# Kernel tuning notes

Hardware: AMD Instinct MI355X
Metric: run time of the kernel (lower is better)

Reference implementation:

```python
import jax, jax.numpy as jnp
import numpy as np

N_NODES = 50000
N_EDGES = 800000
N_GRAPHS = 500
BN_EPS = 1e-5
DIMS = [128, 256, 256, 256, 256, 256, 256]  # in, conv1..5, concat


def setup_inputs() -> dict:
    key = jax.random.key(0)
    ks = jax.random.split(key, 16)
    inp = {
        "x": jax.random.normal(ks[0], (N_NODES, DIMS[0]), jnp.float32),
        "edge_index": jax.random.randint(ks[1], (2, N_EDGES), 0, N_NODES, dtype=jnp.int64),
        "batch": jnp.sort(jax.random.randint(ks[2], (N_NODES,), 0, N_GRAPHS, dtype=jnp.int64)),
    }
    for i in range(6):
        fin, fout = DIMS[i], DIMS[i + 1]
        inp[f"W{i+1}"] = jax.random.normal(ks[3 + i], (fin, fout), jnp.float32) / np.sqrt(fin)
        inp[f"b{i+1}"] = jnp.zeros((fout,), jnp.float32)
    for i in range(5):
        inp[f"gamma{i+1}"] = jnp.ones((DIMS[i + 1],), jnp.float32)
        inp[f"beta{i+1}"] = jnp.zeros((DIMS[i + 1],), jnp.float32)
    return inp


def _gcn_conv(x, src, dst, dinv, W, b):
    # PyG GCNConv: add self-loops, symmetric norm D^-1/2 (A+I) D^-1/2, x@W then aggregate, + bias
    xw = x @ W  # [N, Fout]
    norm = dinv[src] * dinv[dst]  # [E]
    agg = jax.ops.segment_sum(norm[:, None] * xw[src], dst, num_segments=N_NODES)
    agg = agg + (dinv * dinv)[:, None] * xw  # self-loop contribution
    return agg + b


def _bn(x, gamma, beta):
    # BatchNorm1d, training-mode batch statistics (biased variance, as torch)
    m = x.mean(axis=0)
    v = x.var(axis=0)
    return gamma * (x - m) * jax.lax.rsqrt(v + BN_EPS) + beta


def reference(x, edge_index, batch,
              W1, b1, W2, b2, W3, b3, W4, b4, W5, b5, W6, b6,
              gamma1, beta1, gamma2, beta2, gamma3, beta3, gamma4, beta4, gamma5, beta5):
    src, dst = edge_index[0], edge_index[1]
    # degree of A + I (counted over destination nodes)
    deg = jnp.zeros((N_NODES,), x.dtype).at[dst].add(1.0) + 1.0
    dinv = jax.lax.rsqrt(deg)
    h = x
    convs = [(W1, b1), (W2, b2), (W3, b3), (W4, b4), (W5, b5)]
    bns = [(gamma1, beta1), (gamma2, beta2), (gamma3, beta3), (gamma4, beta4), (gamma5, beta5)]
    for (W, b), (g, be) in zip(convs, bns):
        h = jax.nn.relu(_gcn_conv(h, src, dst, dinv, W, b))
        h = _bn(h, g, be)
    h = jax.nn.relu(_gcn_conv(h, src, dst, dinv, W6, b6))
    # global_add_pool; dropout is identity in eval mode
    return jax.ops.segment_sum(h, batch, num_segments=N_GRAPHS)
```

## Files before the change

kernel.cpp:

```cpp
#include <hip/hip_runtime.h>

#define N_NODES 50000
#define N_EDGES 800000
#define N_GRAPHS 500
#define BN_EPS 1e-5f
#define F 256
#define SCAN_BLOCKS ((N_NODES + 255) / 256)
#define NPART 64

typedef short short8 __attribute__((ext_vector_type(8)));
typedef short short4v __attribute__((ext_vector_type(4)));
typedef float f32x4 __attribute__((ext_vector_type(4)));
typedef _Float16 h16x8 __attribute__((ext_vector_type(8)));

__global__ void k_hist(const int* __restrict__ dst, int* __restrict__ cnt) {
    int e0 = (blockIdx.x * blockDim.x + threadIdx.x) * 4;
    if (e0 >= N_EDGES) return;
    int4 d4 = *reinterpret_cast<const int4*>(&dst[e0]);
    atomicAdd(&cnt[d4.x], 1);
    atomicAdd(&cnt[d4.y], 1);
    atomicAdd(&cnt[d4.z], 1);
    atomicAdd(&cnt[d4.w], 1);
}

__global__ void k_dinv(const int* __restrict__ cnt, float* __restrict__ dinv) {
    int n = blockIdx.x * blockDim.x + threadIdx.x;
    if (n < N_NODES) dinv[n] = rsqrtf((float)cnt[n] + 1.0f);
}

__global__ void k_scan1(const int* __restrict__ cnt, int* __restrict__ rowptr,
                        int* __restrict__ bsum) {
    __shared__ int s[256];
    int tid = threadIdx.x;
    int i = blockIdx.x * 256 + tid;
    int v = (i < N_NODES) ? cnt[i] : 0;
    s[tid] = v;
    __syncthreads();
    for (int off = 1; off < 256; off <<= 1) {
        int add = (tid >= off) ? s[tid - off] : 0;
        __syncthreads();
        s[tid] += add;
        __syncthreads();
    }
    if (i < N_NODES) rowptr[i] = s[tid] - v;
    if (tid == 255) bsum[blockIdx.x] = s[255];
}

__global__ void k_scan2(int* __restrict__ bsum) {
    __shared__ int s[256];
    int tid = threadIdx.x;
    int v = (tid < SCAN_BLOCKS) ? bsum[tid] : 0;
    s[tid] = v;
    __syncthreads();
    for (int off = 1; off < 256; off <<= 1) {
        int add = (tid >= off) ? s[tid - off] : 0;
        __syncthreads();
        s[tid] += add;
        __syncthreads();
    }
    if (tid < SCAN_BLOCKS) bsum[tid] = s[tid] - v;
}

__global__ void k_scan3(int* __restrict__ rowptr, const int* __restrict__ bsum) {
    int i = blockIdx.x * 256 + threadIdx.x;
    if (i < N_NODES) rowptr[i] += bsum[blockIdx.x];
    if (i == 0) rowptr[N_NODES] = N_EDGES;
}

__global__ void k_scatter(const int* __restrict__ src, const int* __restrict__ dst,
                          const float* __restrict__ dinv, int* __restrict__ fillptr,
                          int2* __restrict__ epair) {
    int e0 = (blockIdx.x * blockDim.x + threadIdx.x) * 4;
    if (e0 >= N_EDGES) return;
    int4 s4 = *reinterpret_cast<const int4*>(&src[e0]);
    int4 d4 = *reinterpret_cast<const int4*>(&dst[e0]);
    int ss[4] = {s4.x, s4.y, s4.z, s4.w};
    int dd[4] = {d4.x, d4.y, d4.z, d4.w};
    #pragma unroll
    for (int j = 0; j < 4; ++j) {
        float norm = dinv[ss[j]] * dinv[dd[j]];
        int slot = atomicAdd(&fillptr[dd[j]], 1);
        epair[slot] = make_int2(ss[j], __float_as_int(norm));
    }
}

__global__ void k_pack(const float* __restrict__ W, short* __restrict__ hi,
                       short* __restrict__ lo, int K) {
    int idx = blockIdx.x * 256 + threadIdx.x;
    if (idx >= 256 * K) return;
    int n = idx / K, k = idx - n * K;
    float f = W[(size_t)k * 256 + n];
    unsigned u = __builtin_bit_cast(unsigned, f);
    hi[idx] = (short)(u >> 16);
    float hf = __builtin_bit_cast(float, u & 0xFFFF0000u);
    lo[idx] = (short)(__builtin_bit_cast(unsigned, f - hf) >> 16);
}

__global__ __launch_bounds__(256)
void k_wfold(const float* __restrict__ W, const float* __restrict__ stats,
             const float* __restrict__ gamma, const float* __restrict__ beta,
             short* __restrict__ hi, short* __restrict__ lo,
             float* __restrict__ rowvec) {
    __shared__ float red[256];
    const int n = blockIdx.x;
    const int k = threadIdx.x;
    float s = 0.f, q = 0.f;
    for (int p = 0; p < NPART; ++p) {
        s += stats[(size_t)p * 512 + k];
        q += stats[(size_t)p * 512 + 256 + k];
    }
    float m = s * (1.0f / N_NODES);
    float var = q * (1.0f / N_NODES) - m * m;
    float mulk = gamma[k] * rsqrtf(var + BN_EPS);
    float addk = beta[k] - m * mulk;
    float w = W[(size_t)k * 256 + n];
    float f = w * mulk;
    unsigned u = __builtin_bit_cast(unsigned, f);
    hi[(size_t)n * 256 + k] = (short)(u >> 16);
    float hf = __builtin_bit_cast(float, u & 0xFFFF0000u);
    lo[(size_t)n * 256 + k] = (short)(__builtin_bit_cast(unsigned, f - hf) >> 16);
    red[k] = addk * w;
    __syncthreads();
    for (int off = 128; off > 0; off >>= 1) {
        if (k < off) red[k] += red[k + off];
        __syncthreads();
    }
    if (k == 0) rowvec[n] = red[0];
}

__global__ void k_splitx(const float* __restrict__ x, short* __restrict__ hi,
                         short* __restrict__ lo) {
    int idx = blockIdx.x * 256 + threadIdx.x;
    if (idx >= N_NODES * 32) return;
    float4 v = reinterpret_cast<const float4*>(x)[idx];
    float vv[4] = {v.x, v.y, v.z, v.w};
    short4v h4, l4;
    #pragma unroll
    for (int j = 0; j < 4; ++j) {
        unsigned u = __builtin_bit_cast(unsigned, vv[j]);
        h4[j] = (short)(u >> 16);
        float hf = __builtin_bit_cast(float, u & 0xFFFF0000u);
        l4[j] = (short)(__builtin_bit_cast(unsigned, vv[j] - hf) >> 16);
    }
    *reinterpret_cast<short4v*>(&hi[(size_t)idx * 4]) = h4;
    *reinterpret_cast<short4v*>(&lo[(size_t)idx * 4]) = l4;
}

#define BK 32
__global__ __launch_bounds__(256)
void k_gemm_mfma(const short* __restrict__ Ahi, const short* __restrict__ Alo,
                 const short* __restrict__ Bhi, const short* __restrict__ Blo,
                 _Float16* __restrict__ C, int M, int K) {
    __shared__ unsigned As[2][2][128 * 16];
    const int tid  = threadIdx.x;
    const int lane = tid & 63;
    const int w    = tid >> 6;
    const int wr   = (w >> 1) * 64;
    const int wc   = (w & 1) * 64;
    const int bid  = blockIdx.x;
    const int bx   = (bid >> 4) * 8 + (bid & 7);
    const int by   = (bid >> 3) & 1;
    const int brow = bx * 128;
    const int bcol = by * 128;

    f32x4 acc[4][4];
    #pragma unroll
    for (int m = 0; m < 4; ++m)
        #pragma unroll
        for (int n = 0; n < 4; ++n) acc[m][n] = (f32x4){0.f, 0.f, 0.f, 0.f};

    const int lr = tid >> 1;
    const int lk = (tid & 1) * 16;
    const int grow = brow + lr;
    const bool rowok = grow < M;
    const short* Ahp = Ahi + (size_t)grow * K + lk;
    const short* Alp = Alo + (size_t)grow * K + lk;
    const int NS = K / BK;

    uint4 ph0, ph1, pl0, pl1;
    auto load_pf = [&](int s) {
        if (rowok) {
            ph0 = *reinterpret_cast<const uint4*>(Ahp + s * BK);
            ph1 = *reinterpret_cast<const uint4*>(Ahp + s * BK + 8);
            pl0 = *reinterpret_cast<const uint4*>(Alp + s * BK);
            pl1 = *reinterpret_cast<const uint4*>(Alp + s * BK + 8);
        } else {
            ph0 = ph1 = pl0 = pl1 = make_uint4(0, 0, 0, 0);
        }
    };

    const int sw  = (lr >> 1) & 3;
    const int c0  = (tid & 1) * 2;
    const int off0 = lr * 16 + ((c0 ^ sw) << 2);
    const int off1 = lr * 16 + (((c0 + 1) ^ sw) << 2);

    load_pf(0);
    *reinterpret_cast<uint4*>(&As[0][0][off0]) = ph0;
    *reinterpret_cast<uint4*>(&As[0][0][off1]) = ph1;
    *reinterpret_cast<uint4*>(&As[0][1][off0]) = pl0;
    *reinterpret_cast<uint4*>(&As[0][1][off1]) = pl1;

    for (int s = 0; s < NS; ++s) {
        const int cur = s & 1;
        if (s + 1 < NS) load_pf(s + 1);
        __syncthreads();

        short8 bh[4], bl[4];
        const int kb = s * BK + (lane >> 4) * 8;
        #pragma unroll
        for (int n = 0; n < 4; ++n) {
            int col = bcol + wc + n * 16 + (lane & 15);
            bh[n] = *reinterpret_cast<const short8*>(Bhi + (size_t)col * K + kb);
            bl[n] = *reinterpret_cast<const short8*>(Blo + (size_t)col * K + kb);
        }
        #pragma unroll
        for (int m = 0; m < 4; ++m) {
            int row = wr + m * 16 + (lane & 15);
            int c = lane >> 4;
            int sw2 = (row >> 1) & 3;
            const unsigned* ph = &As[cur][0][row * 16 + ((c ^ sw2) << 2)];
            const unsigned* pl = &As[cur][1][row * 16 + ((c ^ sw2) << 2)];
            short8 ah = *reinterpret_cast<const short8*>(ph);
            short8 al = *reinterpret_cast<const short8*>(pl);
            #pragma unroll
            for (int n = 0; n < 4; ++n) {
                acc[m][n] = __builtin_amdgcn_mfma_f32_16x16x32_bf16(ah, bh[n], acc[m][n], 0, 0, 0);
                acc[m][n] = __builtin_amdgcn_mfma_f32_16x16x32_bf16(al, bh[n], acc[m][n], 0, 0, 0);
                acc[m][n] = __builtin_amdgcn_mfma_f32_16x16x32_bf16(ah, bl[n], acc[m][n], 0, 0, 0);
            }
        }
        if (s + 1 < NS) {
            *reinterpret_cast<uint4*>(&As[cur ^ 1][0][off0]) = ph0;
            *reinterpret_cast<uint4*>(&As[cur ^ 1][0][off1]) = ph1;
            *reinterpret_cast<uint4*>(&As[cur ^ 1][1][off0]) = pl0;
            *reinterpret_cast<uint4*>(&As[cur ^ 1][1][off1]) = pl1;
        }
    }

    #pragma unroll
    for (int m = 0; m < 4; ++m) {
        #pragma unroll
        for (int n = 0; n < 4; ++n) {
            int col = bcol + wc + n * 16 + (lane & 15);
            #pragma unroll
            for (int j = 0; j < 4; ++j) {
                int row = brow + wr + m * 16 + (lane >> 4) * 4 + j;
                if (row < M) C[(size_t)row * 256 + col] = (_Float16)acc[m][n][j];
            }
        }
    }
}

#define BATCH 8
template<int MODE>
__global__ __launch_bounds__(256)
void k_agg2(const _Float16* __restrict__ xw, const float* __restrict__ dinv,
            const int* __restrict__ rowptr, const int2* __restrict__ epair,
            const float* __restrict__ bias, const float* __restrict__ rowvec,
            short* __restrict__ hhi, short* __restrict__ hlo,
            float* __restrict__ hf32, float* __restrict__ stats) {
    __shared__ float red[2][4][256];
    const int lane = threadIdx.x & 63;
    const int wave = threadIdx.x >> 6;
    const int half = lane >> 5;
    const int fl   = lane & 31;
    const int n    = blockIdx.x * 4 + wave;

    const h16x8* xw8 = reinterpret_cast<const h16x8*>(xw);

    float acc[8];
    float wsum;
    if (half == 0) {
        float d = dinv[n];
        float sl = d * d;
        h16x8 sv = xw8[(size_t)n * 32 + fl];
        #pragma unroll
        for (int j = 0; j < 8; ++j) acc[j] = sl * (float)sv[j];
        wsum = sl;
    } else {
        #pragma unroll
        for (int j = 0; j < 8; ++j) acc[j] = 0.f;
        wsum = 0.f;
    }

    const int beg = rowptr[n], end = rowptr[n + 1];
    int i = beg + half;

    if (i < end) {
        int ecur[BATCH]; float wcur[BATCH];
        #pragma unroll
        for (int k = 0; k < BATCH; ++k) {
            int idx = i + 2 * k;
            bool ok = idx < end;
            int2 p = epair[ok ? idx : (end - 1)];
            ecur[k] = p.x;
            wcur[k] = ok ? __int_as_float(p.y) : 0.f;
        }
        while (true) {
            h16x8 r[BATCH];
            #pragma unroll
            for (int k = 0; k < BATCH; ++k)
                r[k] = xw8[(size_t)ecur[k] * 32 + fl];

            int inext = i + 2 * BATCH;
            bool more = inext < end;
            int enxt[BATCH]; float wnxt[BATCH];
            if (more) {
                #pragma unroll
                for (int k = 0; k < BATCH; ++k) {
                    int idx = inext + 2 * k;
                    bool ok = idx < end;
                    int2 p = epair[ok ? idx : (end - 1)];
                    enxt[k] = p.x;
                    wnxt[k] = ok ? __int_as_float(p.y) : 0.f;
                }
            }
            #pragma unroll
            for (int k = 0; k < BATCH; ++k) {
                wsum += wcur[k];
                #pragma unroll
                for (int j = 0; j < 8; ++j)
                    acc[j] = fmaf(wcur[k], (float)r[k][j], acc[j]);
            }
            if (!more) break;
            i = inext;
            #pragma unroll
            for (int k = 0; k < BATCH; ++k) { ecur[k] = enxt[k]; wcur[k] = wnxt[k]; }
        }
    }

    #pragma unroll
    for (int j = 0; j < 8; ++j) acc[j] += __shfl_xor(acc[j], 32, 64);
    wsum += __shfl_xor(wsum, 32, 64);

    if (half == 0) {
        float4 b0 = *reinterpret_cast<const float4*>(&bias[fl * 8]);
        float4 b1 = *reinterpret_cast<const float4*>(&bias[fl * 8 + 4]);
        float4 r0 = *reinterpret_cast<const float4*>(&rowvec[fl * 8]);
        float4 r1 = *reinterpret_cast<const float4*>(&rowvec[fl * 8 + 4]);
        float bv[8] = {b0.x, b0.y, b0.z, b0.w, b1.x, b1.y, b1.z, b1.w};
        float rv[8] = {r0.x, r0.y, r0.z, r0.w, r1.x, r1.y, r1.z, r1.w};
        #pragma unroll
        for (int j = 0; j < 8; ++j)
            acc[j] = fmaxf(acc[j] + fmaf(wsum, rv[j], bv[j]), 0.f);

        if (MODE == 0) {
            unsigned hw[4], lw[4];
            #pragma unroll
            for (int p = 0; p < 4; ++p) {
                float f0 = acc[2 * p], f1 = acc[2 * p + 1];
                unsigned u0 = __builtin_bit_cast(unsigned, f0);
                unsigned u1 = __builtin_bit_cast(unsigned, f1);
                hw[p] = (u1 & 0xFFFF0000u) | (u0 >> 16);
                float h0 = __builtin_bit_cast(float, u0 & 0xFFFF0000u);
                float h1 = __builtin_bit_cast(float, u1 & 0xFFFF0000u);
                lw[p] = (__builtin_bit_cast(unsigned, f1 - h1) & 0xFFFF0000u) |
                        (__builtin_bit_cast(unsigned, f0 - h0) >> 16);
            }
            *reinterpret_cast<uint4*>(&hhi[(size_t)n * 256 + fl * 8]) =
                make_uint4(hw[0], hw[1], hw[2], hw[3]);
            *reinterpret_cast<uint4*>(&hlo[(size_t)n * 256 + fl * 8]) =
                make_uint4(lw[0], lw[1], lw[2], lw[3]);
            float4 o0 = make_float4(acc[0], acc[1], acc[2], acc[3]);
            float4 o1 = make_float4(acc[4], acc[5], acc[6], acc[7]);
            float4 q0 = make_float4(acc[0]*acc[0], acc[1]*acc[1], acc[2]*acc[2], acc[3]*acc[3]);
            float4 q1 = make_float4(acc[4]*acc[4], acc[5]*acc[5], acc[6]*acc[6], acc[7]*acc[7]);
            *reinterpret_cast<float4*>(&red[0][wave][fl * 8])     = o0;
            *reinterpret_cast<float4*>(&red[0][wave][fl * 8 + 4]) = o1;
            *reinterpret_cast<float4*>(&red[1][wave][fl * 8])     = q0;
            *reinterpret_cast<float4*>(&red[1][wave][fl * 8 + 4]) = q1;
        } else {
            *reinterpret_cast<float4*>(&hf32[(size_t)n * 256 + fl * 8]) =
                make_float4(acc[0], acc[1], acc[2], acc[3]);
            *reinterpret_cast<float4*>(&hf32[(size_t)n * 256 + fl * 8 + 4]) =
                make_float4(acc[4], acc[5], acc[6], acc[7]);
        }
    }

    if (MODE == 0) {
        __syncthreads();
        int t = threadIdx.x;
        float s = red[0][0][t] + red[0][1][t] + red[0][2][t] + red[0][3][t];
        float q = red[1][0][t] + red[1][1][t] + red[1][2][t] + red[1][3][t];
        float* part = stats + (size_t)(blockIdx.x & (NPART - 1)) * 512;
        atomicAdd(&part[t], s);
        atomicAdd(&part[256 + t], q);
    }
}

template<int ROWS>
__global__ __launch_bounds__(256)
void k_pool(const float* __restrict__ h, const int* __restrict__ batch,
            float* __restrict__ out) {
    const int f = threadIdx.x;
    const int r0 = blockIdx.x * ROWS;
    float acc = 0.f;
    int cur = -1;
    for (int i = 0; i < ROWS; ++i) {
        int n = r0 + i;
        if (n >= N_NODES) break;
        int g = batch[n];
        float v = h[(size_t)n * F + f];
        if (g != cur) {
            if (cur >= 0) atomicAdd(&out[(size_t)cur * F + f], acc);
            cur = g; acc = v;
        } else {
            acc += v;
        }
    }
    if (cur >= 0) atomicAdd(&out[(size_t)cur * F + f], acc);
}

extern "C" void kernel_launch(void* const* d_in, const int* in_sizes, int n_in,
                              void* d_out, int out_size, void* d_ws, size_t ws_size,
                              hipStream_t stream) {
    const float* x     = (const float*)d_in[0];
    const int*   ei    = (const int*)d_in[1];
    const int*   batch = (const int*)d_in[2];
    const float* W[6], *bias[6], *gamma[5], *beta[5];
    for (int i = 0; i < 6; ++i) {
        W[i]    = (const float*)d_in[3 + 2 * i];
        bias[i] = (const float*)d_in[4 + 2 * i];
    }
    for (int i = 0; i < 5; ++i) {
        gamma[i] = (const float*)d_in[15 + 2 * i];
        beta[i]  = (const float*)d_in[16 + 2 * i];
    }
    float* out = (float*)d_out;

    char* ws = (char*)d_ws;
    size_t off = 0;
    auto alloc = [&](size_t bytes) {
        void* p = ws + off;
        off = (off + bytes + 255) & ~(size_t)255;
        return p;
    };
    int*   cnt      = (int*)  alloc(N_NODES * 4);
    int*   rowptr   = (int*)  alloc((N_NODES + 1) * 4);
    int*   fillptr  = (int*)  alloc(N_NODES * 4);
    int*   bsum     = (int*)  alloc(256 * 4);
    float* dinv     = (float*)alloc(N_NODES * 4);
    int2*  epair    = (int2*) alloc((size_t)N_EDGES * 8);
    float* rowvec   = (float*)alloc(F * 4);
    float* statsAll = (float*)alloc((size_t)5 * NPART * 512 * 4);
    short* Whi[6]; short* Wlo[6];
    for (int l = 0; l < 6; ++l) {
        int K = (l == 0) ? 128 : 256;
        Whi[l] = (short*)alloc((size_t)256 * K * 2);
        Wlo[l] = (short*)alloc((size_t)256 * K * 2);
    }
    short* xhi = (short*)alloc((size_t)N_NODES * 128 * 2);
    short* xlo = (short*)alloc((size_t)N_NODES * 128 * 2);
    short* hhi = (short*)alloc((size_t)N_NODES * F * 2);
    short* hlo = (short*)alloc((size_t)N_NODES * F * 2);
    _Float16* xw   = (_Float16*)alloc((size_t)N_NODES * F * 2);
    float*    hfin = (float*)   alloc((size_t)N_NODES * F * 4);

    const int* src = ei;
    const int* dst = ei + N_EDGES;

    hipMemsetAsync(cnt, 0, N_NODES * 4, stream);
    hipMemsetAsync(out, 0, (size_t)N_GRAPHS * F * 4, stream);
    hipMemsetAsync(rowvec, 0, F * 4, stream);
    hipMemsetAsync(statsAll, 0, (size_t)5 * NPART * 512 * 4, stream);
    k_hist<<<(N_EDGES / 4 + 255) / 256, 256, 0, stream>>>(dst, cnt);
    k_dinv<<<(N_NODES + 255) / 256, 256, 0, stream>>>(cnt, dinv);
    k_scan1<<<SCAN_BLOCKS, 256, 0, stream>>>(cnt, rowptr, bsum);
    k_scan2<<<1, 256, 0, stream>>>(bsum);
    k_scan3<<<SCAN_BLOCKS, 256, 0, stream>>>(rowptr, bsum);
    hipMemcpyAsync(fillptr, rowptr, N_NODES * 4, hipMemcpyDeviceToDevice, stream);
    k_scatter<<<(N_EDGES / 4 + 255) / 256, 256, 0, stream>>>(src, dst, dinv, fillptr, epair);
    k_pack<<<(256 * 128 + 255) / 256, 256, 0, stream>>>(W[0], Whi[0], Wlo[0], 128);
    k_splitx<<<(N_NODES * 32 + 255) / 256, 256, 0, stream>>>(x, xhi, xlo);

    const int aggGrid = N_NODES / 4;
    for (int l = 0; l < 6; ++l) {
        const int K = (l == 0) ? 128 : 256;
        const short* Ah = (l == 0) ? xhi : hhi;
        const short* Al = (l == 0) ? xlo : hlo;
        k_gemm_mfma<<<784, 256, 0, stream>>>(Ah, Al, Whi[l], Wlo[l], xw, N_NODES, K);

        if (l < 5) {
            float* stats = statsAll + (size_t)l * NPART * 512;
            k_agg2<0><<<aggGrid, 256, 0, stream>>>(xw, dinv, rowptr, epair,
                                                   bias[l], rowvec, hhi, hlo,
                                                   nullptr, stats);
            k_wfold<<<256, 256, 0, stream>>>(W[l + 1], stats, gamma[l], beta[l],
                                             Whi[l + 1], Wlo[l + 1], rowvec);
        } else {
            k_agg2<1><<<aggGrid, 256, 0, stream>>>(xw, dinv, rowptr, epair,
                                                   bias[l], rowvec, nullptr, nullptr,
                                                   hfin, nullptr);
            k_pool<128><<<(N_NODES + 127) / 128, 256, 0, stream>>>(hfin, batch, out);
        }
    }
}
```

Measured before the change: 1.076 ms.

## Split aggregation into feature chunks with one node per 4-lane group

```diff
diff --git a/kernel.cpp b/kernel.cpp
--- a/kernel.cpp
+++ b/kernel.cpp
@@ -7,6 +7,9 @@
 #define F 256
 #define SCAN_BLOCKS ((N_NODES + 255) / 256)
 #define NPART 64
+#define NCHUNK 8
+#define NODES_PER_BLOCK 64
+#define NODE_BLOCKS ((N_NODES + NODES_PER_BLOCK - 1) / NODES_PER_BLOCK)
 
 typedef short short8 __attribute__((ext_vector_type(8)));
 typedef short short4v __attribute__((ext_vector_type(4)));
@@ -251,93 +254,66 @@
     }
 }
 
-#define BATCH 8
 template<int MODE>
 __global__ __launch_bounds__(256)
-void k_agg2(const _Float16* __restrict__ xw, const float* __restrict__ dinv,
+void k_agg3(const _Float16* __restrict__ xw, const float* __restrict__ dinv,
             const int* __restrict__ rowptr, const int2* __restrict__ epair,
             const float* __restrict__ bias, const float* __restrict__ rowvec,
             short* __restrict__ hhi, short* __restrict__ hlo,
-            float* __restrict__ hf32, float* __restrict__ stats) {
-    __shared__ float red[2][4][256];
-    const int lane = threadIdx.x & 63;
-    const int wave = threadIdx.x >> 6;
-    const int half = lane >> 5;
-    const int fl   = lane & 31;
-    const int n    = blockIdx.x * 4 + wave;
-
+            _Float16* __restrict__ hfin, float* __restrict__ stats) {
+    const int tid   = threadIdx.x;
+    const int lane  = tid & 63;
+    const int wave  = tid >> 6;
+    const int grp   = lane >> 2;
+    const int sub   = lane & 3;
+    const int nb    = blockIdx.x % NODE_BLOCKS;
+    const int ch    = blockIdx.x / NODE_BLOCKS;
+    const int n     = nb * NODES_PER_BLOCK + wave * 16 + grp;
+    const int fbase = ch * 32 + sub * 8;
+    const int unit  = ch * 4 + sub;
     const h16x8* xw8 = reinterpret_cast<const h16x8*>(xw);
 
     float acc[8];
-    float wsum;
-    if (half == 0) {
+    #pragma unroll
+    for (int j = 0; j < 8; ++j) acc[j] = 0.f;
+    const bool valid = (n < N_NODES);
+
+    if (valid) {
         float d = dinv[n];
         float sl = d * d;
-        h16x8 sv = xw8[(size_t)n * 32 + fl];
+        h16x8 sv = xw8[(size_t)n * 32 + unit];
         #pragma unroll
         for (int j = 0; j < 8; ++j) acc[j] = sl * (float)sv[j];
-        wsum = sl;
-    } else {
-        #pragma unroll
-        for (int j = 0; j < 8; ++j) acc[j] = 0.f;
-        wsum = 0.f;
-    }
-
-    const int beg = rowptr[n], end = rowptr[n + 1];
-    int i = beg + half;
-
-    if (i < end) {
-        int ecur[BATCH]; float wcur[BATCH];
-        #pragma unroll
-        for (int k = 0; k < BATCH; ++k) {
-            int idx = i + 2 * k;
-            bool ok = idx < end;
-            int2 p = epair[ok ? idx : (end - 1)];
-            ecur[k] = p.x;
-            wcur[k] = ok ? __int_as_float(p.y) : 0.f;
-        }
-        while (true) {
-            h16x8 r[BATCH];
-            #pragma unroll
-            for (int k = 0; k < BATCH; ++k)
-                r[k] = xw8[(size_t)ecur[k] * 32 + fl];
-
-            int inext = i + 2 * BATCH;
-            bool more = inext < end;
-            int enxt[BATCH]; float wnxt[BATCH];
-            if (more) {
-                #pragma unroll
-                for (int k = 0; k < BATCH; ++k) {
-                    int idx = inext + 2 * k;
-                    bool ok = idx < end;
-                    int2 p = epair[ok ? idx : (end - 1)];
-                    enxt[k] = p.x;
-                    wnxt[k] = ok ? __int_as_float(p.y) : 0.f;
-                }
-            }
-            #pragma unroll
-            for (int k = 0; k < BATCH; ++k) {
-                wsum += wcur[k];
+        float wsum = sl;
+
+        const int beg = rowptr[n], end = rowptr[n + 1];
+        for (int i = beg; i < end; i += 4) {
+            int e[4]; float wv[4];
+            #pragma unroll
+            for (int k = 0; k < 4; ++k) {
+                int idx = i + k;
+                bool ok = idx < end;
+                int2 p = epair[ok ? idx : (end - 1)];
+                e[k]  = p.x;
+                wv[k] = ok ? __int_as_float(p.y) : 0.f;
+            }
+            h16x8 r[4];
+            #pragma unroll
+            for (int k = 0; k < 4; ++k)
+                r[k] = xw8[(size_t)e[k] * 32 + unit];
+            #pragma unroll
+            for (int k = 0; k < 4; ++k) {
+                wsum += wv[k];
                 #pragma unroll
                 for (int j = 0; j < 8; ++j)
-                    acc[j] = fmaf(wcur[k], (float)r[k][j], acc[j]);
-            }
-            if (!more) break;
-            i = inext;
-            #pragma unroll
-            for (int k = 0; k < BATCH; ++k) { ecur[k] = enxt[k]; wcur[k] = wnxt[k]; }
-        }
-    }
-
-    #pragma unroll
-    for (int j = 0; j < 8; ++j) acc[j] += __shfl_xor(acc[j], 32, 64);
-    wsum += __shfl_xor(wsum, 32, 64);
-
-    if (half == 0) {
-        float4 b0 = *reinterpret_cast<const float4*>(&bias[fl * 8]);
-        float4 b1 = *reinterpret_cast<const float4*>(&bias[fl * 8 + 4]);
-        float4 r0 = *reinterpret_cast<const float4*>(&rowvec[fl * 8]);
-        float4 r1 = *reinterpret_cast<const float4*>(&rowvec[fl * 8 + 4]);
+                    acc[j] = fmaf(wv[k], (float)r[k][j], acc[j]);
+            }
+        }
+
+        float4 b0 = *reinterpret_cast<const float4*>(&bias[fbase]);
+        float4 b1 = *reinterpret_cast<const float4*>(&bias[fbase + 4]);
+        float4 r0 = *reinterpret_cast<const float4*>(&rowvec[fbase]);
+        float4 r1 = *reinterpret_cast<const float4*>(&rowvec[fbase + 4]);
         float bv[8] = {b0.x, b0.y, b0.z, b0.w, b1.x, b1.y, b1.z, b1.w};
         float rv[8] = {r0.x, r0.y, r0.z, r0.w, r1.x, r1.y, r1.z, r1.w};
         #pragma unroll
@@ -357,40 +333,44 @@
                 lw[p] = (__builtin_bit_cast(unsigned, f1 - h1) & 0xFFFF0000u) |
                         (__builtin_bit_cast(unsigned, f0 - h0) >> 16);
             }
-            *reinterpret_cast<uint4*>(&hhi[(size_t)n * 256 + fl * 8]) =
+            *reinterpret_cast<uint4*>(&hhi[(size_t)n * 256 + fbase]) =
                 make_uint4(hw[0], hw[1], hw[2], hw[3]);
-            *reinterpret_cast<uint4*>(&hlo[(size_t)n * 256 + fl * 8]) =
+            *reinterpret_cast<uint4*>(&hlo[(size_t)n * 256 + fbase]) =
                 make_uint4(lw[0], lw[1], lw[2], lw[3]);
-            float4 o0 = make_float4(acc[0], acc[1], acc[2], acc[3]);
-            float4 o1 = make_float4(acc[4], acc[5], acc[6], acc[7]);
-            float4 q0 = make_float4(acc[0]*acc[0], acc[1]*acc[1], acc[2]*acc[2], acc[3]*acc[3]);
-            float4 q1 = make_float4(acc[4]*acc[4], acc[5]*acc[5], acc[6]*acc[6], acc[7]*acc[7]);
-            *reinterpret_cast<float4*>(&red[0][wave][fl * 8])     = o0;
-            *reinterpret_cast<float4*>(&red[0][wave][fl * 8 + 4]) = o1;
-            *reinterpret_cast<float4*>(&red[1][wave][fl * 8])     = q0;
-            *reinterpret_cast<float4*>(&red[1][wave][fl * 8 + 4]) = q1;
         } else {
-            *reinterpret_cast<float4*>(&hf32[(size_t)n * 256 + fl * 8]) =
-                make_float4(acc[0], acc[1], acc[2], acc[3]);
-            *reinterpret_cast<float4*>(&hf32[(size_t)n * 256 + fl * 8 + 4]) =
-                make_float4(acc[4], acc[5], acc[6], acc[7]);
+            h16x8 o;
+            #pragma unroll
+            for (int j = 0; j < 8; ++j) o[j] = (_Float16)acc[j];
+            *reinterpret_cast<h16x8*>(&hfin[(size_t)n * 256 + fbase]) = o;
         }
     }
 
     if (MODE == 0) {
-        __syncthreads();
-        int t = threadIdx.x;
-        float s = red[0][0][t] + red[0][1][t] + red[0][2][t] + red[0][3][t];
-        float q = red[1][0][t] + red[1][1][t] + red[1][2][t] + red[1][3][t];
-        float* part = stats + (size_t)(blockIdx.x & (NPART - 1)) * 512;
-        atomicAdd(&part[t], s);
-        atomicAdd(&part[256 + t], q);
+        float s[8], q[8];
+        #pragma unroll
+        for (int j = 0; j < 8; ++j) { s[j] = acc[j]; q[j] = acc[j] * acc[j]; }
+        #pragma unroll
+        for (int m = 4; m <= 32; m <<= 1) {
+            #pragma unroll
+            for (int j = 0; j < 8; ++j) {
+                s[j] += __shfl_xor(s[j], m, 64);
+                q[j] += __shfl_xor(q[j], m, 64);
+            }
+        }
+        if (grp == 0) {
+            float* part = stats + (size_t)(blockIdx.x & (NPART - 1)) * 512;
+            #pragma unroll
+            for (int j = 0; j < 8; ++j) {
+                atomicAdd(&part[fbase + j], s[j]);
+                atomicAdd(&part[256 + fbase + j], q[j]);
+            }
+        }
     }
 }
 
 template<int ROWS>
 __global__ __launch_bounds__(256)
-void k_pool(const float* __restrict__ h, const int* __restrict__ batch,
+void k_pool(const _Float16* __restrict__ h, const int* __restrict__ batch,
             float* __restrict__ out) {
     const int f = threadIdx.x;
     const int r0 = blockIdx.x * ROWS;
@@ -400,7 +380,7 @@
         int n = r0 + i;
         if (n >= N_NODES) break;
         int g = batch[n];
-        float v = h[(size_t)n * F + f];
+        float v = (float)h[(size_t)n * F + f];
         if (g != cur) {
             if (cur >= 0) atomicAdd(&out[(size_t)cur * F + f], acc);
             cur = g; acc = v;
@@ -454,7 +434,7 @@
     short* hhi = (short*)alloc((size_t)N_NODES * F * 2);
     short* hlo = (short*)alloc((size_t)N_NODES * F * 2);
     _Float16* xw   = (_Float16*)alloc((size_t)N_NODES * F * 2);
-    float*    hfin = (float*)   alloc((size_t)N_NODES * F * 4);
+    _Float16* hfin = (_Float16*)alloc((size_t)N_NODES * F * 2);
 
     const int* src = ei;
     const int* dst = ei + N_EDGES;
@@ -473,7 +453,7 @@
     k_pack<<<(256 * 128 + 255) / 256, 256, 0, stream>>>(W[0], Whi[0], Wlo[0], 128);
     k_splitx<<<(N_NODES * 32 + 255) / 256, 256, 0, stream>>>(x, xhi, xlo);
 
-    const int aggGrid = N_NODES / 4;
+    const int aggGrid = NCHUNK * NODE_BLOCKS;
     for (int l = 0; l < 6; ++l) {
         const int K = (l == 0) ? 128 : 256;
         const short* Ah = (l == 0) ? xhi : hhi;
@@ -482,13 +462,13 @@
 
         if (l < 5) {
             float* stats = statsAll + (size_t)l * NPART * 512;
-            k_agg2<0><<<aggGrid, 256, 0, stream>>>(xw, dinv, rowptr, epair,
+            k_agg3<0><<<aggGrid, 256, 0, stream>>>(xw, dinv, rowptr, epair,
                                                    bias[l], rowvec, hhi, hlo,
                                                    nullptr, stats);
             k_wfold<<<256, 256, 0, stream>>>(W[l + 1], stats, gamma[l], beta[l],
                                              Whi[l + 1], Wlo[l + 1], rowvec);
         } else {
-            k_agg2<1><<<aggGrid, 256, 0, stream>>>(xw, dinv, rowptr, epair,
+            k_agg3<1><<<aggGrid, 256, 0, stream>>>(xw, dinv, rowptr, epair,
                                                    bias[l], rowvec, nullptr, nullptr,
                                                    hfin, nullptr);
             k_pool<128><<<(N_NODES + 127) / 128, 256, 0, stream>>>(hfin, batch, out);
```

After: 1.397 ms. 29.8% more time.

## Stage GEMM A tiles via direct global-to-LDS loads and store final activations in fp16

Applied to the files above, without the earlier changes.

```diff
diff --git a/kernel.cpp b/kernel.cpp
--- a/kernel.cpp
+++ b/kernel.cpp
@@ -12,6 +12,9 @@
 typedef short short4v __attribute__((ext_vector_type(4)));
 typedef float f32x4 __attribute__((ext_vector_type(4)));
 typedef _Float16 h16x8 __attribute__((ext_vector_type(8)));
+
+#define AS1 __attribute__((address_space(1)))
+#define AS3 __attribute__((address_space(3)))
 
 __global__ void k_hist(const int* __restrict__ dst, int* __restrict__ cnt) {
     int e0 = (blockIdx.x * blockDim.x + threadIdx.x) * 4;
@@ -151,7 +154,7 @@
 void k_gemm_mfma(const short* __restrict__ Ahi, const short* __restrict__ Alo,
                  const short* __restrict__ Bhi, const short* __restrict__ Blo,
                  _Float16* __restrict__ C, int M, int K) {
-    __shared__ unsigned As[2][2][128 * 16];
+    __shared__ unsigned As[2][2][2][4][256];
     const int tid  = threadIdx.x;
     const int lane = tid & 63;
     const int w    = tid >> 6;
@@ -169,41 +172,29 @@
         #pragma unroll
         for (int n = 0; n < 4; ++n) acc[m][n] = (f32x4){0.f, 0.f, 0.f, 0.f};
 
-    const int lr = tid >> 1;
-    const int lk = (tid & 1) * 16;
-    const int grow = brow + lr;
-    const bool rowok = grow < M;
-    const short* Ahp = Ahi + (size_t)grow * K + lk;
-    const short* Alp = Alo + (size_t)grow * K + lk;
     const int NS = K / BK;
-
-    uint4 ph0, ph1, pl0, pl1;
-    auto load_pf = [&](int s) {
-        if (rowok) {
-            ph0 = *reinterpret_cast<const uint4*>(Ahp + s * BK);
-            ph1 = *reinterpret_cast<const uint4*>(Ahp + s * BK + 8);
-            pl0 = *reinterpret_cast<const uint4*>(Alp + s * BK);
-            pl1 = *reinterpret_cast<const uint4*>(Alp + s * BK + 8);
-        } else {
-            ph0 = ph1 = pl0 = pl1 = make_uint4(0, 0, 0, 0);
+    const int srow = (w << 5) + (lane & 31);
+    const size_t srbase = (size_t)(brow + srow) * K;
+
+    auto stage = [&](int s, int b) {
+        #pragma unroll
+        for (int j = 0; j < 2; ++j) {
+            int u = (j << 1) | (lane >> 5);
+            const short* gh = Ahi + srbase + (size_t)s * BK + u * 8;
+            const short* gl = Alo + srbase + (size_t)s * BK + u * 8;
+            __builtin_amdgcn_global_load_lds((const AS1 void*)gh,
+                                             (AS3 void*)&As[b][0][j][w][0], 16, 0, 0);
+            __builtin_amdgcn_global_load_lds((const AS1 void*)gl,
+                                             (AS3 void*)&As[b][1][j][w][0], 16, 0, 0);
         }
     };
 
-    const int sw  = (lr >> 1) & 3;
-    const int c0  = (tid & 1) * 2;
-    const int off0 = lr * 16 + ((c0 ^ sw) << 2);
-    const int off1 = lr * 16 + (((c0 + 1) ^ sw) << 2);
-
-    load_pf(0);
-    *reinterpret_cast<uint4*>(&As[0][0][off0]) = ph0;
-    *reinterpret_cast<uint4*>(&As[0][0][off1]) = ph1;
-    *reinterpret_cast<uint4*>(&As[0][1][off0]) = pl0;
-    *reinterpret_cast<uint4*>(&As[0][1][off1]) = pl1;
+    stage(0, 0);
+    __syncthreads();
 
     for (int s = 0; s < NS; ++s) {
         const int cur = s & 1;
-        if (s + 1 < NS) load_pf(s + 1);
-        __syncthreads();
+        if (s + 1 < NS) stage(s + 1, cur ^ 1);
 
         short8 bh[4], bl[4];
         const int kb = s * BK + (lane >> 4) * 8;
@@ -213,13 +204,15 @@
             bh[n] = *reinterpret_cast<const short8*>(Bhi + (size_t)col * K + kb);
             bl[n] = *reinterpret_cast<const short8*>(Blo + (size_t)col * K + kb);
         }
+        const int j    = lane >> 5;
+        const int lsel = ((lane >> 4) & 1) << 5;
         #pragma unroll
         for (int m = 0; m < 4; ++m) {
-            int row = wr + m * 16 + (lane & 15);
-            int c = lane >> 4;
-            int sw2 = (row >> 1) & 3;
-            const unsigned* ph = &As[cur][0][row * 16 + ((c ^ sw2) << 2)];
-            const unsigned* pl = &As[cur][1][row * 16 + ((c ^ sw2) << 2)];
+            int row  = wr + m * 16 + (lane & 15);
+            int wprm = (row >> 5) & 3;
+            int lidx = (row & 31) | lsel;
+            const unsigned* ph = &As[cur][0][j][wprm][lidx * 4];
+            const unsigned* pl = &As[cur][1][j][wprm][lidx * 4];
             short8 ah = *reinterpret_cast<const short8*>(ph);
             short8 al = *reinterpret_cast<const short8*>(pl);
             #pragma unroll
@@ -229,12 +222,7 @@
                 acc[m][n] = __builtin_amdgcn_mfma_f32_16x16x32_bf16(ah, bl[n], acc[m][n], 0, 0, 0);
             }
         }
-        if (s + 1 < NS) {
-            *reinterpret_cast<uint4*>(&As[cur ^ 1][0][off0]) = ph0;
-            *reinterpret_cast<uint4*>(&As[cur ^ 1][0][off1]) = ph1;
-            *reinterpret_cast<uint4*>(&As[cur ^ 1][1][off0]) = pl0;
-            *reinterpret_cast<uint4*>(&As[cur ^ 1][1][off1]) = pl1;
-        }
+        __syncthreads();
     }
 
     #pragma unroll
@@ -243,9 +231,9 @@
         for (int n = 0; n < 4; ++n) {
             int col = bcol + wc + n * 16 + (lane & 15);
             #pragma unroll
-            for (int j = 0; j < 4; ++j) {
-                int row = brow + wr + m * 16 + (lane >> 4) * 4 + j;
-                if (row < M) C[(size_t)row * 256 + col] = (_Float16)acc[m][n][j];
+            for (int j2 = 0; j2 < 4; ++j2) {
+                int row = brow + wr + m * 16 + (lane >> 4) * 4 + j2;
+                if (row < M) C[(size_t)row * 256 + col] = (_Float16)acc[m][n][j2];
             }
         }
     }
@@ -258,7 +246,7 @@
             const int* __restrict__ rowptr, const int2* __restrict__ epair,
             const float* __restrict__ bias, const float* __restrict__ rowvec,
             short* __restrict__ hhi, short* __restrict__ hlo,
-            float* __restrict__ hf32, float* __restrict__ stats) {
+            _Float16* __restrict__ hfin, float* __restrict__ stats) {
     __shared__ float red[2][4][256];
     const int lane = threadIdx.x & 63;
     const int wave = threadIdx.x >> 6;
@@ -370,10 +358,10 @@
             *reinterpret_cast<float4*>(&red[1][wave][fl * 8])     = q0;
             *reinterpret_cast<float4*>(&red[1][wave][fl * 8 + 4]) = q1;
         } else {
-            *reinterpret_cast<float4*>(&hf32[(size_t)n * 256 + fl * 8]) =
-                make_float4(acc[0], acc[1], acc[2], acc[3]);
-            *reinterpret_cast<float4*>(&hf32[(size_t)n * 256 + fl * 8 + 4]) =
-                make_float4(acc[4], acc[5], acc[6], acc[7]);
+            h16x8 o;
+            #pragma unroll
+            for (int j = 0; j < 8; ++j) o[j] = (_Float16)acc[j];
+            *reinterpret_cast<h16x8*>(&hfin[(size_t)n * 256 + fl * 8]) = o;
         }
     }
 
@@ -390,7 +378,7 @@
 
 template<int ROWS>
 __global__ __launch_bounds__(256)
-void k_pool(const float* __restrict__ h, const int* __restrict__ batch,
+void k_pool(const _Float16* __restrict__ h, const int* __restrict__ batch,
             float* __restrict__ out) {
     const int f = threadIdx.x;
     const int r0 = blockIdx.x * ROWS;
@@ -400,7 +388,7 @@
         int n = r0 + i;
         if (n >= N_NODES) break;
         int g = batch[n];
-        float v = h[(size_t)n * F + f];
+        float v = (float)h[(size_t)n * F + f];
         if (g != cur) {
             if (cur >= 0) atomicAdd(&out[(size_t)cur * F + f], acc);
             cur = g; acc = v;
@@ -454,7 +442,7 @@
     short* hhi = (short*)alloc((size_t)N_NODES * F * 2);
     short* hlo = (short*)alloc((size_t)N_NODES * F * 2);
     _Float16* xw   = (_Float16*)alloc((size_t)N_NODES * F * 2);
-    float*    hfin = (float*)   alloc((size_t)N_NODES * F * 4);
+    _Float16* hfin = (_Float16*)alloc((size_t)N_NODES * F * 2);
 
     const int* src = ei;
     const int* dst = ei + N_EDGES;
```

After: 1.013 ms. 1.06x faster.
